# Performance work log

Hardware: AMD Instinct MI355X
Metric: run time of the kernel (lower is better)

## Reference

```python
import jax, jax.numpy as jnp
import numpy as np

BATCH, CLASSES = 32768, 1000
SMOOTHING = 0.1  # timm-style LabelSmoothingCrossEntropy default


def setup_inputs() -> dict:
    key = jax.random.key(0)
    k1, k2 = jax.random.split(key)
    output = jax.random.normal(k1, (BATCH, CLASSES), dtype=jnp.float32)
    target = jax.random.randint(k2, (BATCH,), 0, CLASSES, dtype=jnp.int64)
    return {"output": output, "target": target}


def _label_smoothing_ce(x, target, smoothing=SMOOTHING):
    # timm-style: loss = (1-eps)*NLL + eps*mean(-logp)
    logp = jax.nn.log_softmax(x, axis=-1)
    nll = -jnp.take_along_axis(logp, target[:, None], axis=-1)[:, 0]
    smooth = -logp.mean(axis=-1)
    return ((1.0 - smoothing) * nll + smoothing * smooth).mean()


def reference(output, target):
    batch, classes = output.shape
    probs = jax.nn.softmax(output, axis=1)  # [B, C]
    # per-class empirical frequency via one-pass bincount
    counts = jnp.zeros((classes,), dtype=probs.dtype).at[target].add(1.0)
    avg_count = counts / batch                 # [C]
    avg_conf = probs.mean(axis=0)              # [C]
    loss_mdca = jnp.abs(avg_conf - avg_count).sum() / classes
    # faithful to original: label-smoothing CE applied to softmaxed output
    loss_ce = _label_smoothing_ce(probs, target)
    loss = loss_ce + loss_mdca
    return (loss, loss_ce, loss_mdca)
```

## Files before the change

### kernel.cpp

```cpp
#include <hip/hip_runtime.h>
#include <math.h>

#define BATCH   32768
#define CLASSES 1000
#define EPS     0.1f

#define MB   256
#define MT   1024
#define WPB  16
#define NPROC (MB * WPB)
#define ROWS_PER_WAVE (BATCH / NPROC)
#define ILP   4
#define OUTER (ROWS_PER_WAVE / ILP)

#define PSTRIDE   2048
#define PARTIAL_F 0
#define SPART_F   (MB * PSTRIDE)
#define ACC_F     (SPART_F + 2 * MB)

__global__ __launch_bounds__(MT)
void mdca_main(const float* __restrict__ x, const int* __restrict__ target,
               float* __restrict__ partial, float* __restrict__ spart,
               float* __restrict__ acc) {
    __shared__ float cs[WPB][1024];
    __shared__ float cnt[1024];
    __shared__ float red[2][WPB];

    const int tid  = threadIdx.x;
    const int wave = tid >> 6;
    const int lane = tid & 63;

    if (blockIdx.x == 0 && tid == 0) { acc[0] = 0.f; acc[1] = 0.f; }

    float4* my4 = reinterpret_cast<float4*>(cs[wave]);
    #pragma unroll
    for (int k = 0; k < 4; ++k) my4[64 * k + lane] = make_float4(0.f, 0.f, 0.f, 0.f);
    cnt[tid] = 0.f;
    __syncthreads();

    const int proc = blockIdx.x * WPB + __builtin_amdgcn_readfirstlane(wave);
    float acc_l = 0.f, acc_p = 0.f;

    #pragma unroll
    for (int outer = 0; outer < OUTER; ++outer) {
        int    r[ILP], t[ILP];
        float4 v[ILP][4];
        #pragma unroll
        for (int s = 0; s < ILP; ++s) r[s] = proc + (outer * ILP + s) * NPROC;
        #pragma unroll
        for (int s = 0; s < ILP; ++s) t[s] = target[r[s]];
        #pragma unroll
        for (int s = 0; s < ILP; ++s) {
            const float4* row4 = reinterpret_cast<const float4*>(x + (size_t)r[s] * CLASSES);
            #pragma unroll
            for (int k = 0; k < 4; ++k) {
                const int idx4 = 64 * k + lane;
                v[s][k] = (idx4 < CLASSES / 4)
                        ? row4[idx4]
                        : make_float4(-INFINITY, -INFINITY, -INFINITY, -INFINITY);
            }
        }

        float z[ILP], et[ILP];
        #pragma unroll
        for (int s = 0; s < ILP; ++s) {
            float zl = 0.f, el = 0.f;
            #pragma unroll
            for (int k = 0; k < 4; ++k) {
                float4 e;
                e.x = __expf(v[s][k].x); e.y = __expf(v[s][k].y);
                e.z = __expf(v[s][k].z); e.w = __expf(v[s][k].w);
                v[s][k] = e;
                zl += (e.x + e.y) + (e.z + e.w);
                const int d = t[s] - 4 * (64 * k + lane);
                if ((unsigned)d < 4u)
                    el += (d == 0) ? e.x : (d == 1) ? e.y : (d == 2) ? e.z : e.w;
            }
            z[s] = zl; et[s] = el;
        }
        #pragma unroll
        for (int o = 32; o > 0; o >>= 1) {
            #pragma unroll
            for (int s = 0; s < ILP; ++s) {
                z[s]  += __shfl_xor(z[s],  o, 64);
                et[s] += __shfl_xor(et[s], o, 64);
            }
        }

        float iz[ILP], s2[ILP];
        #pragma unroll
        for (int s = 0; s < ILP; ++s) { iz[s] = 1.0f / z[s]; s2[s] = 0.f; }

        #pragma unroll
        for (int k = 0; k < 4; ++k) {
            const int idx4 = 64 * k + lane;
            const bool valid = idx4 < CLASSES / 4;
            float4 col = make_float4(0.f, 0.f, 0.f, 0.f);
            #pragma unroll
            for (int s = 0; s < ILP; ++s) {
                float4 p;
                p.x = v[s][k].x * iz[s]; p.y = v[s][k].y * iz[s];
                p.z = v[s][k].z * iz[s]; p.w = v[s][k].w * iz[s];
                if (valid)
                    s2[s] += (__expf(p.x) + __expf(p.y)) + (__expf(p.z) + __expf(p.w));
                col.x += p.x; col.y += p.y; col.z += p.z; col.w += p.w;
            }
            if (valid) {
                float4 o4 = my4[idx4];
                o4.x += col.x; o4.y += col.y; o4.z += col.z; o4.w += col.w;
                my4[idx4] = o4;
            }
        }
        #pragma unroll
        for (int o = 32; o > 0; o >>= 1) {
            #pragma unroll
            for (int s = 0; s < ILP; ++s) s2[s] += __shfl_xor(s2[s], o, 64);
        }
        #pragma unroll
        for (int s = 0; s < ILP; ++s) {
            acc_l += __logf(s2[s]);
            acc_p += et[s] * iz[s];
        }
        if (lane == 0) {
            #pragma unroll
            for (int s = 0; s < ILP; ++s) atomicAdd(&cnt[t[s]], 1.0f);
        }
    }

    if (lane == 0) { red[0][wave] = acc_l; red[1][wave] = acc_p; }
    __syncthreads();

    float* pslice = partial + (size_t)blockIdx.x * PSTRIDE;
    if (tid < CLASSES) {
        float s = 0.f;
        #pragma unroll
        for (int w = 0; w < WPB; ++w) s += cs[w][tid];
        pslice[tid]        = s;
        pslice[1024 + tid] = cnt[tid];
    }
    if (tid == 0) {
        float sl = 0.f, sp = 0.f;
        for (int w = 0; w < WPB; ++w) { sl += red[0][w]; sp += red[1][w]; }
        spart[2 * blockIdx.x]     = sl;
        spart[2 * blockIdx.x + 1] = sp;
    }
}

__global__ __launch_bounds__(128)
void mdca_finish(const float* __restrict__ partial, const float* __restrict__ spart,
                 float* __restrict__ acc, float* __restrict__ out) {
    const int tid  = threadIdx.x;
    const int wave = tid >> 6;
    const int lane = tid & 63;
    const int col  = blockIdx.x * 128 + tid;

    float conf = 0.f, c2 = 0.f;
    #pragma unroll 8
    for (int b = 0; b < MB; ++b) {
        conf += partial[(size_t)b * PSTRIDE + col];
        c2   += partial[(size_t)b * PSTRIDE + 1024 + col];
    }
    float d = (col < CLASSES) ? fabsf(conf - c2) * (1.0f / BATCH) : 0.f;

    float sl = spart[2 * tid]     + spart[2 * (tid + 128)];
    float sp = spart[2 * tid + 1] + spart[2 * (tid + 128) + 1];

    #pragma unroll
    for (int o = 32; o > 0; o >>= 1) {
        d  += __shfl_xor(d,  o, 64);
        sl += __shfl_xor(sl, o, 64);
        sp += __shfl_xor(sp, o, 64);
    }
    __shared__ float sred[3][2];
    if (lane == 0) { sred[0][wave] = d; sred[1][wave] = sl; sred[2][wave] = sp; }
    __syncthreads();

    if (tid == 0) {
        const float dtot = sred[0][0] + sred[0][1];
        atomicAdd(&acc[0], dtot);
        __threadfence();
        const unsigned tk = atomicAdd((unsigned int*)&acc[1], 1u);
        if (tk == gridDim.x - 1) {
            __threadfence();
            const float mdca = atomicAdd(&acc[0], 0.0f) * (1.0f / CLASSES);
            const float slt  = sred[1][0] + sred[1][1];
            const float spt  = sred[2][0] + sred[2][1];
            const float ce = slt * (1.0f / BATCH)
                           - (1.0f - EPS) * (spt * (1.0f / BATCH))
                           - EPS / CLASSES;
            out[0] = ce + mdca;
            out[1] = ce;
            out[2] = mdca;
        }
    }
}

extern "C" void kernel_launch(void* const* d_in, const int* in_sizes, int n_in,
                              void* d_out, int out_size, void* d_ws, size_t ws_size,
                              hipStream_t stream) {
    const float* x   = (const float*)d_in[0];
    const int*   tgt = (const int*)d_in[1];
    float* out = (float*)d_out;
    float* ws  = (float*)d_ws;

    mdca_main<<<MB, MT, 0, stream>>>(x, tgt, ws + PARTIAL_F, ws + SPART_F, ws + ACC_F);
    mdca_finish<<<8, 128, 0, stream>>>(ws + PARTIAL_F, ws + SPART_F, ws + ACC_F, out);
}
```

Baseline: 223.8 us.

## Restructure finish kernel into two-stage parallel reduction with last-block ticket

The finish kernel is changed from 8 blocks of 128 threads, each serially summing 256 partial rows, to 16 blocks of 1024 threads. Each block sums a 32-row slice for one column half and writes the result to a stage2 buffer. A ticket atomic then picks the last block, which folds the 8 stage2 rows and the scalar partials and writes the outputs. The aim is to cut the latency of the long serial column loop in the small finish launch. In exchange it adds an extra global round-trip and a grid-wide fence handshake.

```diff
diff --git a/kernel.cpp b/kernel.cpp
--- a/kernel.cpp
+++ b/kernel.cpp
@@ -13,15 +13,18 @@
 #define ILP   4
 #define OUTER (ROWS_PER_WAVE / ILP)
 
+#define FBLK 16
+
 #define PSTRIDE   2048
 #define PARTIAL_F 0
 #define SPART_F   (MB * PSTRIDE)
-#define ACC_F     (SPART_F + 2 * MB)
+#define STAGE2_F  (SPART_F + 1024)
+#define TICKET_F  (STAGE2_F + 8 * PSTRIDE)
 
 __global__ __launch_bounds__(MT)
 void mdca_main(const float* __restrict__ x, const int* __restrict__ target,
                float* __restrict__ partial, float* __restrict__ spart,
-               float* __restrict__ acc) {
+               float* __restrict__ ticket) {
     __shared__ float cs[WPB][1024];
     __shared__ float cnt[1024];
     __shared__ float red[2][WPB];
@@ -30,7 +33,7 @@
     const int wave = tid >> 6;
     const int lane = tid & 63;
 
-    if (blockIdx.x == 0 && tid == 0) { acc[0] = 0.f; acc[1] = 0.f; }
+    if (blockIdx.x == 0 && tid == 0) ((unsigned int*)ticket)[0] = 0u;
 
     float4* my4 = reinterpret_cast<float4*>(cs[wave]);
     #pragma unroll
@@ -146,24 +149,42 @@
     }
 }
 
-__global__ __launch_bounds__(128)
+__global__ __launch_bounds__(1024)
 void mdca_finish(const float* __restrict__ partial, const float* __restrict__ spart,
-                 float* __restrict__ acc, float* __restrict__ out) {
+                 float* __restrict__ stage2, float* __restrict__ ticket,
+                 float* __restrict__ out) {
     const int tid  = threadIdx.x;
     const int wave = tid >> 6;
     const int lane = tid & 63;
-    const int col  = blockIdx.x * 128 + tid;
+    const int cg   = blockIdx.x & 1;
+    const int rg   = blockIdx.x >> 1;
+    const int col  = cg * 1024 + tid;
+
+    float s = 0.f;
+    #pragma unroll
+    for (int r = 0; r < 32; ++r)
+        s += partial[(size_t)(rg * 32 + r) * PSTRIDE + col];
+    stage2[rg * PSTRIDE + col] = s;
+
+    __threadfence();
+    __syncthreads();
+    __shared__ int is_last;
+    if (tid == 0)
+        is_last = (atomicAdd((unsigned int*)ticket, 1u) == FBLK - 1);
+    __syncthreads();
+    if (!is_last) return;
+    __threadfence();
 
     float conf = 0.f, c2 = 0.f;
-    #pragma unroll 8
-    for (int b = 0; b < MB; ++b) {
-        conf += partial[(size_t)b * PSTRIDE + col];
-        c2   += partial[(size_t)b * PSTRIDE + 1024 + col];
-    }
-    float d = (col < CLASSES) ? fabsf(conf - c2) * (1.0f / BATCH) : 0.f;
-
-    float sl = spart[2 * tid]     + spart[2 * (tid + 128)];
-    float sp = spart[2 * tid + 1] + spart[2 * (tid + 128) + 1];
+    #pragma unroll
+    for (int g = 0; g < 8; ++g) {
+        conf += stage2[g * PSTRIDE + tid];
+        c2   += stage2[g * PSTRIDE + 1024 + tid];
+    }
+    float d = (tid < CLASSES) ? fabsf(conf - c2) * (1.0f / BATCH) : 0.f;
+
+    float sl = (tid < MB) ? spart[2 * tid]     : 0.f;
+    float sp = (tid < MB) ? spart[2 * tid + 1] : 0.f;
 
     #pragma unroll
     for (int o = 32; o > 0; o >>= 1) {
@@ -171,27 +192,21 @@
         sl += __shfl_xor(sl, o, 64);
         sp += __shfl_xor(sp, o, 64);
     }
-    __shared__ float sred[3][2];
+    __shared__ float sred[3][16];
     if (lane == 0) { sred[0][wave] = d; sred[1][wave] = sl; sred[2][wave] = sp; }
     __syncthreads();
 
     if (tid == 0) {
-        const float dtot = sred[0][0] + sred[0][1];
-        atomicAdd(&acc[0], dtot);
-        __threadfence();
-        const unsigned tk = atomicAdd((unsigned int*)&acc[1], 1u);
-        if (tk == gridDim.x - 1) {
-            __threadfence();
-            const float mdca = atomicAdd(&acc[0], 0.0f) * (1.0f / CLASSES);
-            const float slt  = sred[1][0] + sred[1][1];
-            const float spt  = sred[2][0] + sred[2][1];
-            const float ce = slt * (1.0f / BATCH)
-                           - (1.0f - EPS) * (spt * (1.0f / BATCH))
-                           - EPS / CLASSES;
-            out[0] = ce + mdca;
-            out[1] = ce;
-            out[2] = mdca;
-        }
+        float dt = 0.f, slt = 0.f, spt = 0.f;
+        #pragma unroll
+        for (int w = 0; w < 16; ++w) { dt += sred[0][w]; slt += sred[1][w]; spt += sred[2][w]; }
+        const float mdca = dt / CLASSES;
+        const float ce = slt * (1.0f / BATCH)
+                       - (1.0f - EPS) * (spt * (1.0f / BATCH))
+                       - EPS / CLASSES;
+        out[0] = ce + mdca;
+        out[1] = ce;
+        out[2] = mdca;
     }
 }
 
@@ -203,6 +218,7 @@
     float* out = (float*)d_out;
     float* ws  = (float*)d_ws;
 
-    mdca_main<<<MB, MT, 0, stream>>>(x, tgt, ws + PARTIAL_F, ws + SPART_F, ws + ACC_F);
-    mdca_finish<<<8, 128, 0, stream>>>(ws + PARTIAL_F, ws + SPART_F, ws + ACC_F, out);
+    mdca_main<<<MB, MT, 0, stream>>>(x, tgt, ws + PARTIAL_F, ws + SPART_F, ws + TICKET_F);
+    mdca_finish<<<FBLK, 1024, 0, stream>>>(ws + PARTIAL_F, ws + SPART_F,
+                                           ws + STAGE2_F, ws + TICKET_F, out);
 }
```

Measured after the change: 208.1 us. 7.0% less time.
